# Kernel optimization log

Hardware: AMD Instinct MI355X
Metric: run time of the kernel (lower is better)

The kernel has to match this reference:

```python
import jax, jax.numpy as jnp
import numpy as np

B, N, E, D = 4, 4096, 4096, 128
NEG_SLOPE = 0.01
BN_EPS = 1e-5


def setup_inputs() -> dict:
    key = jax.random.key(0)
    ks = jax.random.split(key, 8)
    return {
        "incident_mat": (jax.random.uniform(ks[0], (B, N, E)) < 0.01).astype(jnp.float32),
        "degree_v": jax.random.normal(ks[1], (B, N, N), jnp.float32) * 0.01,
        "degree_e": jax.random.normal(ks[2], (B, E, E), jnp.float32) * 0.01,
        "x": jax.random.normal(ks[3], (B, N, D), jnp.float32),
        "e_masks": jax.random.randint(ks[4], (B, E), 0, 2, jnp.int32),
        "mlp_W": jax.random.normal(ks[5], (D, D), jnp.float32) / np.sqrt(D),
        "mlp_b": jnp.zeros((D,), jnp.float32),
        "theta_att": jax.random.normal(ks[6], (D, 1), jnp.float32) / np.sqrt(D),
        "eps": jax.random.uniform(ks[7], (1,), jnp.float32),
        "bn_gamma": jnp.ones((D,), jnp.float32),
        "bn_beta": jnp.zeros((D,), jnp.float32),
        "bn_mean": jnp.zeros((D,), jnp.float32),
        "bn_var": jnp.ones((D,), jnp.float32),
    }


def reference(incident_mat, degree_v, degree_e, x, e_masks, mlp_W, mlp_b,
              theta_att, eps, bn_gamma, bn_beta, bn_mean, bn_var):
    # MLP (num_mlp_layers=1 -> single Linear)
    x_w = x @ mlp_W + mlp_b                      # [B,N,D]
    Ht = jnp.swapaxes(incident_mat, 1, 2)        # [B,E,N]
    ht_x_w = Ht @ x_w                            # [B,E,D]
    # attention logits per hyperedge
    ht_x_theta = (Ht @ (x @ theta_att))[..., 0]  # [B,E]
    scores = jnp.where(e_masks == 0, -jnp.inf, ht_x_theta)
    attn = jax.nn.softmax(scores, axis=1)        # [B,E]
    # diag_embed + bmm == elementwise row scaling
    h1 = attn[..., None] * ht_x_w                # [B,E,D]
    h1 = incident_mat @ h1                       # [B,N,D]
    h1 = degree_v @ h1                           # [B,N,D]
    h1 = Ht @ h1                                 # [B,E,D]
    h1 = degree_e @ h1                           # [B,E,D]
    h = h1 + eps * ht_x_w                        # [B,E,D]
    h = incident_mat @ h                         # [B,N,D]
    h = jnp.where(h >= 0, h, NEG_SLOPE * h)      # leaky_relu; dropout=identity (eval)
    # BatchNorm1d over channels (inference mode)
    h = (h - bn_mean) / jnp.sqrt(bn_var + BN_EPS) * bn_gamma + bn_beta
    return h
```

## Files before the change

### kernel.cpp

```cpp
#include <hip/hip_runtime.h>


typedef __bf16 bf16;
typedef bf16 bf16x8 __attribute__((ext_vector_type(8)));
typedef float f32x4 __attribute__((ext_vector_type(4)));
typedef unsigned long long u64;

#define LDK 72
#define SWZ(r, c) ((c) ^ ((((r) >> 3) & 7) << 3))
#define CAP 192

union BPack { bf16 h[2]; unsigned int u; };
static __device__ __forceinline__ bf16 tob(float f) { return (bf16)f; }

__global__ __launch_bounds__(256) void mlp_k(const float* __restrict__ x,
                                             const float* __restrict__ W,
                                             const float* __restrict__ bias,
                                             const float* __restrict__ theta,
                                             float* __restrict__ xw,
                                             float* __restrict__ xt) {
    __shared__ float Ws[32][128];
    __shared__ float xs[32][128];
    const int t = threadIdx.x;
    const long r0 = (long)blockIdx.x * 32;

    for (int i = t * 4; i < 4096; i += 1024)
        *(float4*)&xs[i >> 7][i & 127] = *(const float4*)&x[r0 * 128 + i];

    const int d = t & 127;
    const int rg = (t >> 7) * 16;
    float acc[16];
#pragma unroll
    for (int r = 0; r < 16; ++r) acc[r] = 0.f;

    for (int kk = 0; kk < 128; kk += 32) {
        __syncthreads();
        for (int i = t * 4; i < 4096; i += 1024)
            *(float4*)&Ws[i >> 7][i & 127] =
                *(const float4*)&W[(kk + (i >> 7)) * 128 + (i & 127)];
        __syncthreads();
        for (int k = 0; k < 32; ++k) {
            float w = Ws[k][d];
#pragma unroll
            for (int r = 0; r < 16; ++r) acc[r] += xs[rg + r][kk + k] * w;
        }
    }
    const float bd = bias[d];
#pragma unroll
    for (int r = 0; r < 16; ++r)
        xw[(r0 + rg + r) * 128 + d] = acc[r] + bd;

    if (t < 32) {
        float s = 0.f;
        for (int k = 0; k < 128; ++k) s += xs[t][k] * theta[k];
        xt[r0 + t] = s;
    }
}

__global__ __launch_bounds__(256) void bmask2_k(const float* __restrict__ inc,
                                                u64* __restrict__ rowmask) {
    const int b = blockIdx.y;
    const int n = blockIdx.x * 4 + (threadIdx.x >> 6);
    const int l = threadIdx.x & 63;
    const float* p = inc + ((long)b << 24) + (long)n * 4096 + l * 64;
    u64 w = 0;
#pragma unroll
    for (int j = 0; j < 16; ++j) {
        const float4 v = *(const float4*)(p + j * 4);
        w |= (u64)(v.x != 0.f ? 1u : 0u) << (4 * j);
        w |= (u64)(v.y != 0.f ? 1u : 0u) << (4 * j + 1);
        w |= (u64)(v.z != 0.f ? 1u : 0u) << (4 * j + 2);
        w |= (u64)(v.w != 0.f ? 1u : 0u) << (4 * j + 3);
    }
    rowmask[((long)b * 4096 + n) * 64 + l] = w;
}

__global__ void btrans_k(const u64* __restrict__ rowmask, u64* __restrict__ colmask) {
    const int tn = blockIdx.x, te = blockIdx.y, b = blockIdx.z;
    const int l = threadIdx.x;
    __shared__ u64 w[64];
    w[l] = rowmask[((long)b * 4096 + tn * 64 + l) * 64 + te];
    __syncthreads();
    u64 o = 0;
#pragma unroll 8
    for (int j = 0; j < 64; ++j) o |= ((w[j] >> l) & 1ull) << j;
    colmask[((long)b * 4096 + te * 64 + l) * 64 + tn] = o;
}

__global__ __launch_bounds__(256) void lists_k(const u64* __restrict__ mask,
                                               ushort* __restrict__ idx,
                                               int* __restrict__ cnts) {
    const int b = blockIdx.y;
    const int r = blockIdx.x * 4 + (threadIdx.x >> 6);
    const int l = threadIdx.x & 63;
    u64 m = mask[((long)b * 4096 + r) * 64 + l];
    const int pc = __popcll(m);
    int pre = pc;
#pragma unroll
    for (int o = 1; o < 64; o <<= 1) {
        int t = __shfl_up(pre, o);
        if (l >= o) pre += t;
    }
    const int total = __shfl(pre, 63);
    if (l == 63) cnts[b * 4096 + r] = total;
    ushort* op = idx + ((long)b * 4096 + r) * CAP;
    int k = pre - pc;
    while (m) {
        const int bit = __builtin_ctzll(m);
        m &= m - 1;
        if (k < CAP) op[k] = (ushort)(l * 64 + bit);
        ++k;
    }
}

__global__ void softmax_k(const float* __restrict__ sc, const int* __restrict__ mask,
                          float* __restrict__ attn) {
    const int b = blockIdx.x, t = threadIdx.x;
    __shared__ float red[1024];
    const float* sb = sc + b * 4096;
    const int* mb = mask + b * 4096;

    float mx = -1e30f;
    for (int e = t; e < 4096; e += 1024)
        if (mb[e] != 0) mx = fmaxf(mx, sb[e]);
    red[t] = mx;
    __syncthreads();
    for (int st = 512; st > 0; st >>= 1) {
        if (t < st) red[t] = fmaxf(red[t], red[t + st]);
        __syncthreads();
    }
    mx = red[0];
    __syncthreads();

    float sum = 0.f;
    for (int e = t; e < 4096; e += 1024)
        if (mb[e] != 0) sum += expf(sb[e] - mx);
    red[t] = sum;
    __syncthreads();
    for (int st = 512; st > 0; st >>= 1) {
        if (t < st) red[t] += red[t + st];
        __syncthreads();
    }
    const float inv = 1.f / red[0];
    for (int e = t; e < 4096; e += 1024)
        attn[b * 4096 + e] = (mb[e] != 0) ? expf(sb[e] - mx) * inv : 0.f;
}

__global__ __launch_bounds__(256) void pairsum_k(const float* __restrict__ P,
                                                 float* __restrict__ O) {
    const long i4 = (long)blockIdx.x * 256 + threadIdx.x;
    float4 a = ((const float4*)P)[i4];
    float4 c = ((const float4*)P)[i4 + 524288];
    a.x += c.x; a.y += c.y; a.z += c.z; a.w += c.w;
    ((float4*)O)[i4] = a;
}

template <bool SCALE, bool ADDEPS, bool HXT, bool EPI>
__global__ __launch_bounds__(256) void gatherE_k(
    const ushort* __restrict__ idx, const int* __restrict__ cnts,
    const u64* __restrict__ mask, const float* __restrict__ src,
    const float* __restrict__ src2, const float* __restrict__ attn,
    const float* __restrict__ xt, const float* __restrict__ epsp,
    const float* __restrict__ bng, const float* __restrict__ bnb,
    const float* __restrict__ bnm, const float* __restrict__ bnv,
    float* __restrict__ out, float* __restrict__ hxt) {
    const int bid = blockIdx.x;
    const int slot = bid & 7;
    const int b = slot >> 1;
    const int chunk = (bid >> 3) * 2 + (slot & 1);
    const int r = chunk * 4 + (threadIdx.x >> 6);
    const int l = threadIdx.x & 63;
    const long rowid = (long)b * 4096 + r;
    const int cnt = cnts[rowid];
    const ushort* ip = idx + rowid * CAP;
    const float* S = src + (long)b * 524288;
    const float* S2 = ADDEPS ? (src2 + (long)b * 524288) : nullptr;
    const float* ab = attn + (long)b * 4096;
    const float* xb = xt + (long)b * 4096;
    const float eps_v = ADDEPS ? epsp[0] : 0.f;
    const int c0 = 2 * l;

    float a0x = 0.f, a0y = 0.f, a1x = 0.f, a1y = 0.f;
    float a2x = 0.f, a2y = 0.f, a3x = 0.f, a3y = 0.f;
    float hacc = 0.f;

    auto edge1 = [&](int e) {
        float2 v = *(const float2*)(S + (long)e * 128 + c0);
        if (ADDEPS) {
            float2 u = *(const float2*)(S2 + (long)e * 128 + c0);
            v.x += eps_v * u.x; v.y += eps_v * u.y;
        }
        if (SCALE) {
            const float s = ab[e];
            v.x *= s; v.y *= s;
        }
        if (HXT) hacc += xb[e];
        a0x += v.x; a0y += v.y;
    };

    const int n = cnt < CAP ? cnt : CAP;
    int i = 0;
    for (; i + 4 <= n; i += 4) {
        const int e0 = ip[i], e1 = ip[i + 1], e2 = ip[i + 2], e3 = ip[i + 3];
        float2 v0 = *(const float2*)(S + (long)e0 * 128 + c0);
        float2 v1 = *(const float2*)(S + (long)e1 * 128 + c0);
        float2 v2 = *(const float2*)(S + (long)e2 * 128 + c0);
        float2 v3 = *(const float2*)(S + (long)e3 * 128 + c0);
        if (ADDEPS) {
            float2 u0 = *(const float2*)(S2 + (long)e0 * 128 + c0);
            float2 u1 = *(const float2*)(S2 + (long)e1 * 128 + c0);
            float2 u2 = *(const float2*)(S2 + (long)e2 * 128 + c0);
            float2 u3 = *(const float2*)(S2 + (long)e3 * 128 + c0);
            v0.x += eps_v * u0.x; v0.y += eps_v * u0.y;
            v1.x += eps_v * u1.x; v1.y += eps_v * u1.y;
            v2.x += eps_v * u2.x; v2.y += eps_v * u2.y;
            v3.x += eps_v * u3.x; v3.y += eps_v * u3.y;
        }
        if (SCALE) {
            const float s0 = ab[e0], s1 = ab[e1], s2 = ab[e2], s3 = ab[e3];
            v0.x *= s0; v0.y *= s0; v1.x *= s1; v1.y *= s1;
            v2.x *= s2; v2.y *= s2; v3.x *= s3; v3.y *= s3;
        }
        if (HXT) hacc += (xb[e0] + xb[e1]) + (xb[e2] + xb[e3]);
        a0x += v0.x; a0y += v0.y; a1x += v1.x; a1y += v1.y;
        a2x += v2.x; a2y += v2.y; a3x += v3.x; a3y += v3.y;
    }
    for (; i < n; ++i) edge1(ip[i]);

    if (cnt > CAP) {
        const u64 wrd = mask[rowid * 64 + l];
        int seen = 0;
        for (int wi = 0; wi < 64; ++wi) {
            u64 m = __shfl(wrd, wi);
            const int pc = __popcll(m);
            if (seen + pc > CAP) {
                int tk = CAP - seen;
                if (tk < 0) tk = 0;
                for (int t = 0; t < tk; ++t) m &= m - 1;
                while (m) {
                    const int bit = __builtin_ctzll(m);
                    m &= m - 1;
                    edge1((wi << 6) + bit);
                }
            }
            seen += pc;
        }
    }

    float ax = (a0x + a1x) + (a2x + a3x);
    float ay = (a0y + a1y) + (a2y + a3y);
    if (EPI) {
        float t0 = (ax >= 0.f) ? ax : 0.01f * ax;
        float t1 = (ay >= 0.f) ? ay : 0.01f * ay;
        ax = (t0 - bnm[c0]) * rsqrtf(bnv[c0] + 1e-5f) * bng[c0] + bnb[c0];
        ay = (t1 - bnm[c0 + 1]) * rsqrtf(bnv[c0 + 1] + 1e-5f) * bng[c0 + 1] + bnb[c0 + 1];
    }
    *(float2*)&out[(long)b * 524288 + (long)r * 128 + c0] = (float2){ax, ay};
    if (HXT && l == 0) hxt[rowid] = hacc;
}

template <int KS>
__global__ __launch_bounds__(1024, 4) void gemm_dense(
    const float* __restrict__ A, const float* __restrict__ Bsrc,
    float* __restrict__ P) {
    __shared__ __align__(16) bf16 As[2][128][LDK];
    __shared__ __align__(16) bf16 Bs[2][128][LDK];

    const int tid = threadIdx.x;
    const int bid = blockIdx.x;
    const int slot = bid & 7;
    const int b = slot >> 1;
    const int sub = (bid >> 3) * 2 + (slot & 1);
    const int ksi = sub % KS;
    const int m0 = (sub / KS) * 128;
    constexpr int KCH = 4096 / KS;
    const int kbeg = ksi * KCH, kend = kbeg + KCH;
    const long Aoff = (long)b << 24;
    const long Boff = (long)b * 524288;

    const int wave = tid >> 6, lane = tid & 63;
    const int lr = lane & 15, kb = lane >> 4;
    const int wm = (wave >> 2) * 32, wn = (wave & 3) * 32;

    const int ar = tid >> 3, ak = (tid & 7) * 8;
    const int bd4 = (tid & 31) * 4, bk2 = (tid >> 5) * 2;

    const float* Abase = A + Aoff + (long)(m0 + ar) * 4096 + ak;
    const float* Bbase = Bsrc + Boff + (long)bk2 * 128 + bd4;

    f32x4 acc[2][2];
#pragma unroll
    for (int mf = 0; mf < 2; ++mf)
#pragma unroll
        for (int nf = 0; nf < 2; ++nf) acc[mf][nf] = (f32x4){0.f, 0.f, 0.f, 0.f};

    float4 pa0A, pa1A, pb0A, pb1A;
    float4 pa0B, pa1B, pb0B, pb1B;

#define GLOAD(S, kk)                                                        \
    {                                                                       \
        const float* ga = Abase + (kk);                                     \
        pa0##S = *(const float4*)ga;                                        \
        pa1##S = *(const float4*)(ga + 4);                                  \
        const float* gb = Bbase + (long)(kk) * 128;                         \
        pb0##S = *(const float4*)gb;                                        \
        pb1##S = *(const float4*)(gb + 128);                                \
    }

#define STAGE(S, bu)                                                        \
    {                                                                       \
        bf16x8 p;                                                           \
        p[0] = tob(pa0##S.x); p[1] = tob(pa0##S.y); p[2] = tob(pa0##S.z); p[3] = tob(pa0##S.w); \
        p[4] = tob(pa1##S.x); p[5] = tob(pa1##S.y); p[6] = tob(pa1##S.z); p[7] = tob(pa1##S.w); \
        *(bf16x8*)&As[bu][ar][SWZ(ar, ak)] = p;                             \
        float va[4] = {pb0##S.x, pb0##S.y, pb0##S.z, pb0##S.w};             \
        float vb[4] = {pb1##S.x, pb1##S.y, pb1##S.z, pb1##S.w};             \
        _Pragma("unroll")                                                   \
        for (int j = 0; j < 4; ++j) {                                       \
            BPack q; q.h[0] = tob(va[j]); q.h[1] = tob(vb[j]);              \
            *(unsigned int*)&Bs[bu][bd4 + j][SWZ(bd4 + j, bk2)] = q.u;      \
        }                                                                   \
    }

#define MFMA_STEP(bu)                                                       \
    {                                                                       \
        _Pragma("unroll")                                                   \
        for (int ks = 0; ks < 2; ++ks) {                                    \
            const int ka = ks * 32 + kb * 8;                                \
            bf16x8 af[2], bfr[2];                                           \
            _Pragma("unroll")                                               \
            for (int mf = 0; mf < 2; ++mf) {                                \
                const int rA = wm + mf * 16 + lr;                           \
                af[mf] = *(const bf16x8*)&As[bu][rA][SWZ(rA, ka)];          \
            }                                                               \
            _Pragma("unroll")                                               \
            for (int nf = 0; nf < 2; ++nf) {                                \
                const int rB = wn + nf * 16 + lr;                           \
                bfr[nf] = *(const bf16x8*)&Bs[bu][rB][SWZ(rB, ka)];         \
            }                                                               \
            _Pragma("unroll")                                               \
            for (int mf = 0; mf < 2; ++mf)                                  \
                _Pragma("unroll")                                           \
                for (int nf = 0; nf < 2; ++nf)                              \
                    acc[mf][nf] = __builtin_amdgcn_mfma_f32_16x16x32_bf16(  \
                        af[mf], bfr[nf], acc[mf][nf], 0, 0, 0);             \
        }                                                                   \
    }

    GLOAD(A, kbeg);
    GLOAD(B, kbeg + 64);
    STAGE(A, 0);
    __syncthreads();

    for (int kk = kbeg; kk < kend; kk += 128) {
        MFMA_STEP(0);
        STAGE(B, 1);
        if (kk + 128 < kend) GLOAD(A, kk + 128);
        __syncthreads();
        MFMA_STEP(1);
        if (kk + 128 < kend) {
            STAGE(A, 0);
            if (kk + 192 < kend) GLOAD(B, kk + 192);
            __syncthreads();
        }
    }
#undef GLOAD
#undef STAGE
#undef MFMA_STEP

    float* Cp = P + (long)(ksi * 4 + b) * 524288;
#pragma unroll
    for (int mf = 0; mf < 2; ++mf) {
        const int rb = m0 + wm + mf * 16 + kb * 4;
#pragma unroll
        for (int nf = 0; nf < 2; ++nf) {
            const int col = wn + nf * 16 + lr;
#pragma unroll
            for (int i = 0; i < 4; ++i)
                Cp[(long)(rb + i) * 128 + col] = acc[mf][nf][i];
        }
    }
}

template <int KS>
static void run_all(const float* incident, const float* degree_v, const float* degree_e,
                    const float* x, const int* e_masks, const float* mlp_W,
                    const float* mlp_b, const float* theta, const float* epsp,
                    const float* bng, const float* bnb, const float* bnm,
                    const float* bnv, float* out, float* ws, hipStream_t stream) {
    float* xw  = ws;
    float* hxw = ws + 2097152;
    float* t1  = ws + 4194304;
    float* Pd  = ws + 6291456;
    float* Psum = Pd + (long)KS * 2097152;
    float* tail = Psum + 2097152;
    u64* rowmask = (u64*)tail;
    u64* colmask = rowmask + 1048576;
    ushort* rowidx = (ushort*)(colmask + 1048576);
    ushort* colidx = rowidx + 16384 * CAP;
    int* rowcnt = (int*)(colidx + 16384 * CAP);
    int* colcnt = rowcnt + 16384;
    float* xt  = (float*)(colcnt + 16384);
    float* hxt = xt + 16384;
    float* att = hxt + 16384;

    mlp_k<<<512, 256, 0, stream>>>(x, mlp_W, mlp_b, theta, xw, xt);
    bmask2_k<<<dim3(1024, 4), 256, 0, stream>>>(incident, rowmask);
    btrans_k<<<dim3(64, 64, 4), 64, 0, stream>>>(rowmask, colmask);
    lists_k<<<dim3(1024, 4), 256, 0, stream>>>(rowmask, rowidx, rowcnt);
    lists_k<<<dim3(1024, 4), 256, 0, stream>>>(colmask, colidx, colcnt);

    gatherE_k<false, false, true, false><<<4096, 256, 0, stream>>>(
        colidx, colcnt, colmask, xw, nullptr, att, xt, nullptr,
        nullptr, nullptr, nullptr, nullptr, hxw, hxt);
    softmax_k<<<4, 1024, 0, stream>>>(hxt, e_masks, att);
    gatherE_k<true, false, false, false><<<4096, 256, 0, stream>>>(
        rowidx, rowcnt, rowmask, hxw, nullptr, att, xt, nullptr,
        nullptr, nullptr, nullptr, nullptr, t1, nullptr);
    gemm_dense<KS><<<32 * KS * 4, 1024, 0, stream>>>(degree_v, t1, Pd);
    const float* g4src = Pd;
    if (KS == 2) { pairsum_k<<<2048, 256, 0, stream>>>(Pd, Psum); g4src = Psum; }
    gatherE_k<false, false, false, false><<<4096, 256, 0, stream>>>(
        colidx, colcnt, colmask, g4src, nullptr, att, xt, nullptr,
        nullptr, nullptr, nullptr, nullptr, t1, nullptr);
    gemm_dense<KS><<<32 * KS * 4, 1024, 0, stream>>>(degree_e, t1, Pd);
    const float* g6src = Pd;
    if (KS == 2) { pairsum_k<<<2048, 256, 0, stream>>>(Pd, Psum); g6src = Psum; }
    gatherE_k<false, true, false, true><<<4096, 256, 0, stream>>>(
        rowidx, rowcnt, rowmask, g6src, hxw, att, xt, epsp,
        bng, bnb, bnm, bnv, out, nullptr);
}

extern "C" void kernel_launch(void* const* d_in, const int* in_sizes, int n_in,
                              void* d_out, int out_size, void* d_ws, size_t ws_size,
                              hipStream_t stream) {
    const float* incident = (const float*)d_in[0];
    const float* degree_v = (const float*)d_in[1];
    const float* degree_e = (const float*)d_in[2];
    const float* x        = (const float*)d_in[3];
    const int*   e_masks  = (const int*)d_in[4];
    const float* mlp_W    = (const float*)d_in[5];
    const float* mlp_b    = (const float*)d_in[6];
    const float* theta    = (const float*)d_in[7];
    const float* epsp     = (const float*)d_in[8];
    const float* bng      = (const float*)d_in[9];
    const float* bnb      = (const float*)d_in[10];
    const float* bnm      = (const float*)d_in[11];
    const float* bnv      = (const float*)d_in[12];
    float* out = (float*)d_out;
    float* ws = (float*)d_ws;

    if (ws_size >= 95000000ull)
        run_all<2>(incident, degree_v, degree_e, x, e_masks, mlp_W, mlp_b, theta,
                   epsp, bng, bnb, bnm, bnv, out, ws, stream);
    else
        run_all<1>(incident, degree_v, degree_e, x, e_masks, mlp_W, mlp_b, theta,
                   epsp, bng, bnb, bnm, bnv, out, ws, stream);
}
```

Baseline: 431.1 us.

## Fuse row-list build into mask kernel and hoist scaling and eps out of gathers

Builds the row index lists inside the mask kernel, so the separate lists pass and its rowmask reread go away. The per-edge attention scaling and eps*hxw add move out of the gather kernels into dense elementwise passes (a new scale kernel and a pairsum kernel that also adds eps), so every gather reads a single source with no extra per-element loads. The gather loop now loads eight indices at once as a vector, keeps eight independent accumulators and prefetches the next index batch. The cost is extra launches and a larger workspace; the threshold for the split-K path is raised to match, which could change which path runs for some workspace sizes.

```diff
diff --git a/kernel.cpp b/kernel.cpp
--- a/kernel.cpp
+++ b/kernel.cpp
@@ -5,6 +5,8 @@
 typedef bf16 bf16x8 __attribute__((ext_vector_type(8)));
 typedef float f32x4 __attribute__((ext_vector_type(4)));
 typedef unsigned long long u64;
+typedef unsigned short u16;
+typedef u16 u16x8 __attribute__((ext_vector_type(8)));
 
 #define LDK 72
 #define SWZ(r, c) ((c) ^ ((((r) >> 3) & 7) << 3))
@@ -57,8 +59,10 @@
     }
 }
 
-__global__ __launch_bounds__(256) void bmask2_k(const float* __restrict__ inc,
-                                                u64* __restrict__ rowmask) {
+__global__ __launch_bounds__(256) void bmask_lists_k(const float* __restrict__ inc,
+                                                     u64* __restrict__ rowmask,
+                                                     u16* __restrict__ idx,
+                                                     int* __restrict__ cnts) {
     const int b = blockIdx.y;
     const int n = blockIdx.x * 4 + (threadIdx.x >> 6);
     const int l = threadIdx.x & 63;
@@ -72,7 +76,26 @@
         w |= (u64)(v.z != 0.f ? 1u : 0u) << (4 * j + 2);
         w |= (u64)(v.w != 0.f ? 1u : 0u) << (4 * j + 3);
     }
-    rowmask[((long)b * 4096 + n) * 64 + l] = w;
+    const long rowid = (long)b * 4096 + n;
+    rowmask[rowid * 64 + l] = w;
+
+    const int pc = __popcll(w);
+    int pre = pc;
+#pragma unroll
+    for (int o = 1; o < 64; o <<= 1) {
+        int t = __shfl_up(pre, o);
+        if (l >= o) pre += t;
+    }
+    if (l == 63) cnts[rowid] = pre;
+    u16* op = idx + rowid * CAP;
+    int k = pre - pc;
+    u64 m = w;
+    while (m) {
+        const int bit = __builtin_ctzll(m);
+        m &= m - 1;
+        if (k < CAP) op[k] = (u16)(l * 64 + bit);
+        ++k;
+    }
 }
 
 __global__ void btrans_k(const u64* __restrict__ rowmask, u64* __restrict__ colmask) {
@@ -88,7 +111,7 @@
 }
 
 __global__ __launch_bounds__(256) void lists_k(const u64* __restrict__ mask,
-                                               ushort* __restrict__ idx,
+                                               u16* __restrict__ idx,
                                                int* __restrict__ cnts) {
     const int b = blockIdx.y;
     const int r = blockIdx.x * 4 + (threadIdx.x >> 6);
@@ -101,14 +124,13 @@
         int t = __shfl_up(pre, o);
         if (l >= o) pre += t;
     }
-    const int total = __shfl(pre, 63);
-    if (l == 63) cnts[b * 4096 + r] = total;
-    ushort* op = idx + ((long)b * 4096 + r) * CAP;
+    if (l == 63) cnts[b * 4096 + r] = pre;
+    u16* op = idx + ((long)b * 4096 + r) * CAP;
     int k = pre - pc;
     while (m) {
         const int bit = __builtin_ctzll(m);
         m &= m - 1;
-        if (k < CAP) op[k] = (ushort)(l * 64 + bit);
+        if (k < CAP) op[k] = (u16)(l * 64 + bit);
         ++k;
     }
 }
@@ -146,21 +168,40 @@
         attn[b * 4096 + e] = (mb[e] != 0) ? expf(sb[e] - mx) * inv : 0.f;
 }
 
+__global__ __launch_bounds__(256) void scale_k(const float* __restrict__ hxw,
+                                               const float* __restrict__ att,
+                                               float* __restrict__ outp) {
+    const long i4 = (long)blockIdx.x * 256 + threadIdx.x;
+    float4 v = ((const float4*)hxw)[i4];
+    const float s = att[i4 >> 5];
+    v.x *= s; v.y *= s; v.z *= s; v.w *= s;
+    ((float4*)outp)[i4] = v;
+}
+
+template <int KSP, bool EPS>
 __global__ __launch_bounds__(256) void pairsum_k(const float* __restrict__ P,
+                                                 const float* __restrict__ H,
+                                                 const float* __restrict__ epsp,
                                                  float* __restrict__ O) {
     const long i4 = (long)blockIdx.x * 256 + threadIdx.x;
     float4 a = ((const float4*)P)[i4];
-    float4 c = ((const float4*)P)[i4 + 524288];
-    a.x += c.x; a.y += c.y; a.z += c.z; a.w += c.w;
+    if (KSP == 2) {
+        float4 c = ((const float4*)P)[i4 + 524288];
+        a.x += c.x; a.y += c.y; a.z += c.z; a.w += c.w;
+    }
+    if (EPS) {
+        const float e = epsp[0];
+        float4 h = ((const float4*)H)[i4];
+        a.x += e * h.x; a.y += e * h.y; a.z += e * h.z; a.w += e * h.w;
+    }
     ((float4*)O)[i4] = a;
 }
 
-template <bool SCALE, bool ADDEPS, bool HXT, bool EPI>
+template <bool HXT, bool EPI>
 __global__ __launch_bounds__(256) void gatherE_k(
-    const ushort* __restrict__ idx, const int* __restrict__ cnts,
+    const u16* __restrict__ idx, const int* __restrict__ cnts,
     const u64* __restrict__ mask, const float* __restrict__ src,
-    const float* __restrict__ src2, const float* __restrict__ attn,
-    const float* __restrict__ xt, const float* __restrict__ epsp,
+    const float* __restrict__ xt,
     const float* __restrict__ bng, const float* __restrict__ bnb,
     const float* __restrict__ bnm, const float* __restrict__ bnv,
     float* __restrict__ out, float* __restrict__ hxt) {
@@ -172,60 +213,51 @@
     const int l = threadIdx.x & 63;
     const long rowid = (long)b * 4096 + r;
     const int cnt = cnts[rowid];
-    const ushort* ip = idx + rowid * CAP;
+    const u16* ip = idx + rowid * CAP;
     const float* S = src + (long)b * 524288;
-    const float* S2 = ADDEPS ? (src2 + (long)b * 524288) : nullptr;
-    const float* ab = attn + (long)b * 4096;
     const float* xb = xt + (long)b * 4096;
-    const float eps_v = ADDEPS ? epsp[0] : 0.f;
     const int c0 = 2 * l;
 
-    float a0x = 0.f, a0y = 0.f, a1x = 0.f, a1y = 0.f;
-    float a2x = 0.f, a2y = 0.f, a3x = 0.f, a3y = 0.f;
+    float ax0 = 0.f, ax1 = 0.f, ax2 = 0.f, ax3 = 0.f;
+    float ax4 = 0.f, ax5 = 0.f, ax6 = 0.f, ax7 = 0.f;
+    float ay0 = 0.f, ay1 = 0.f, ay2 = 0.f, ay3 = 0.f;
+    float ay4 = 0.f, ay5 = 0.f, ay6 = 0.f, ay7 = 0.f;
     float hacc = 0.f;
-
-    auto edge1 = [&](int e) {
-        float2 v = *(const float2*)(S + (long)e * 128 + c0);
-        if (ADDEPS) {
-            float2 u = *(const float2*)(S2 + (long)e * 128 + c0);
-            v.x += eps_v * u.x; v.y += eps_v * u.y;
-        }
-        if (SCALE) {
-            const float s = ab[e];
-            v.x *= s; v.y *= s;
-        }
-        if (HXT) hacc += xb[e];
-        a0x += v.x; a0y += v.y;
-    };
 
     const int n = cnt < CAP ? cnt : CAP;
     int i = 0;
-    for (; i + 4 <= n; i += 4) {
-        const int e0 = ip[i], e1 = ip[i + 1], e2 = ip[i + 2], e3 = ip[i + 3];
-        float2 v0 = *(const float2*)(S + (long)e0 * 128 + c0);
-        float2 v1 = *(const float2*)(S + (long)e1 * 128 + c0);
-        float2 v2 = *(const float2*)(S + (long)e2 * 128 + c0);
-        float2 v3 = *(const float2*)(S + (long)e3 * 128 + c0);
-        if (ADDEPS) {
-            float2 u0 = *(const float2*)(S2 + (long)e0 * 128 + c0);
-            float2 u1 = *(const float2*)(S2 + (long)e1 * 128 + c0);
-            float2 u2 = *(const float2*)(S2 + (long)e2 * 128 + c0);
-            float2 u3 = *(const float2*)(S2 + (long)e3 * 128 + c0);
-            v0.x += eps_v * u0.x; v0.y += eps_v * u0.y;
-            v1.x += eps_v * u1.x; v1.y += eps_v * u1.y;
-            v2.x += eps_v * u2.x; v2.y += eps_v * u2.y;
-            v3.x += eps_v * u3.x; v3.y += eps_v * u3.y;
+    if (n >= 8) {
+        u16x8 ia = *(const u16x8*)ip;
+        for (; i + 8 <= n; i += 8) {
+            const int e0 = ia[0], e1 = ia[1], e2 = ia[2], e3 = ia[3];
+            const int e4 = ia[4], e5 = ia[5], e6 = ia[6], e7 = ia[7];
+            const float2 v0 = *(const float2*)(S + (long)e0 * 128 + c0);
+            const float2 v1 = *(const float2*)(S + (long)e1 * 128 + c0);
+            const float2 v2 = *(const float2*)(S + (long)e2 * 128 + c0);
+            const float2 v3 = *(const float2*)(S + (long)e3 * 128 + c0);
+            const float2 v4 = *(const float2*)(S + (long)e4 * 128 + c0);
+            const float2 v5 = *(const float2*)(S + (long)e5 * 128 + c0);
+            const float2 v6 = *(const float2*)(S + (long)e6 * 128 + c0);
+            const float2 v7 = *(const float2*)(S + (long)e7 * 128 + c0);
+            const bool more = (i + 16 <= n);
+            u16x8 ib;
+            if (more) ib = *(const u16x8*)(ip + i + 8);
+            if (HXT)
+                hacc += ((xb[e0] + xb[e1]) + (xb[e2] + xb[e3])) +
+                        ((xb[e4] + xb[e5]) + (xb[e6] + xb[e7]));
+            ax0 += v0.x; ay0 += v0.y; ax1 += v1.x; ay1 += v1.y;
+            ax2 += v2.x; ay2 += v2.y; ax3 += v3.x; ay3 += v3.y;
+            ax4 += v4.x; ay4 += v4.y; ax5 += v5.x; ay5 += v5.y;
+            ax6 += v6.x; ay6 += v6.y; ax7 += v7.x; ay7 += v7.y;
+            if (more) ia = ib;
         }
-        if (SCALE) {
-            const float s0 = ab[e0], s1 = ab[e1], s2 = ab[e2], s3 = ab[e3];
-            v0.x *= s0; v0.y *= s0; v1.x *= s1; v1.y *= s1;
-            v2.x *= s2; v2.y *= s2; v3.x *= s3; v3.y *= s3;
-        }
-        if (HXT) hacc += (xb[e0] + xb[e1]) + (xb[e2] + xb[e3]);
-        a0x += v0.x; a0y += v0.y; a1x += v1.x; a1y += v1.y;
-        a2x += v2.x; a2y += v2.y; a3x += v3.x; a3y += v3.y;
-    }
-    for (; i < n; ++i) edge1(ip[i]);
+    }
+    for (; i < n; ++i) {
+        const int e = ip[i];
+        const float2 v = *(const float2*)(S + (long)e * 128 + c0);
+        if (HXT) hacc += xb[e];
+        ax0 += v.x; ay0 += v.y;
+    }
 
     if (cnt > CAP) {
         const u64 wrd = mask[rowid * 64 + l];
@@ -240,15 +272,18 @@
                 while (m) {
                     const int bit = __builtin_ctzll(m);
                     m &= m - 1;
-                    edge1((wi << 6) + bit);
+                    const int e = (wi << 6) + bit;
+                    const float2 v = *(const float2*)(S + (long)e * 128 + c0);
+                    if (HXT) hacc += xb[e];
+                    ax0 += v.x; ay0 += v.y;
                 }
             }
             seen += pc;
         }
     }
 
-    float ax = (a0x + a1x) + (a2x + a3x);
-    float ay = (a0y + a1y) + (a2y + a3y);
+    float ax = ((ax0 + ax1) + (ax2 + ax3)) + ((ax4 + ax5) + (ax6 + ax7));
+    float ay = ((ay0 + ay1) + (ay2 + ay3)) + ((ay4 + ay5) + (ay6 + ay7));
     if (EPI) {
         float t0 = (ax >= 0.f) ? ax : 0.01f * ax;
         float t1 = (ay >= 0.f) ? ay : 0.01f * ay;
@@ -388,16 +423,17 @@
                     const float* mlp_b, const float* theta, const float* epsp,
                     const float* bng, const float* bnb, const float* bnm,
                     const float* bnv, float* out, float* ws, hipStream_t stream) {
-    float* xw  = ws;
-    float* hxw = ws + 2097152;
-    float* t1  = ws + 4194304;
-    float* Pd  = ws + 6291456;
-    float* Psum = Pd + (long)KS * 2097152;
-    float* tail = Psum + 2097152;
+    float* xw    = ws;
+    float* hxw   = ws + 2097152;
+    float* hxw_s = ws + 4194304;
+    float* t1    = ws + 6291456;
+    float* Pd    = ws + 8388608;
+    float* Psum  = Pd + (long)KS * 2097152;
+    float* tail  = Psum + 2097152;
     u64* rowmask = (u64*)tail;
     u64* colmask = rowmask + 1048576;
-    ushort* rowidx = (ushort*)(colmask + 1048576);
-    ushort* colidx = rowidx + 16384 * CAP;
+    u16* rowidx = (u16*)(colmask + 1048576);
+    u16* colidx = rowidx + 16384 * CAP;
     int* rowcnt = (int*)(colidx + 16384 * CAP);
     int* colcnt = rowcnt + 16384;
     float* xt  = (float*)(colcnt + 16384);
@@ -405,30 +441,27 @@
     float* att = hxt + 16384;
 
     mlp_k<<<512, 256, 0, stream>>>(x, mlp_W, mlp_b, theta, xw, xt);
-    bmask2_k<<<dim3(1024, 4), 256, 0, stream>>>(incident, rowmask);
+    bmask_lists_k<<<dim3(1024, 4), 256, 0, stream>>>(incident, rowmask, rowidx, rowcnt);
     btrans_k<<<dim3(64, 64, 4), 64, 0, stream>>>(rowmask, colmask);
-    lists_k<<<dim3(1024, 4), 256, 0, stream>>>(rowmask, rowidx, rowcnt);
     lists_k<<<dim3(1024, 4), 256, 0, stream>>>(colmask, colidx, colcnt);
 
-    gatherE_k<false, false, true, false><<<4096, 256, 0, stream>>>(
-        colidx, colcnt, colmask, xw, nullptr, att, xt, nullptr,
-        nullptr, nullptr, nullptr, nullptr, hxw, hxt);
+    gatherE_k<true, false><<<4096, 256, 0, stream>>>(
+        colidx, colcnt, colmask, xw, xt, nullptr, nullptr, nullptr, nullptr,
+        hxw, hxt);
     softmax_k<<<4, 1024, 0, stream>>>(hxt, e_masks, att);
-    gatherE_k<true, false, false, false><<<4096, 256, 0, stream>>>(
-        rowidx, rowcnt, rowmask, hxw, nullptr, att, xt, nullptr,
-        nullptr, nullptr, nullptr, nullptr, t1, nullptr);
+    scale_k<<<2048, 256, 0, stream>>>(hxw, att, hxw_s);
+    gatherE_k<false, false><<<4096, 256, 0, stream>>>(
+        rowidx, rowcnt, rowmask, hxw_s, xt, nullptr, nullptr, nullptr, nullptr,
+        t1, nullptr);
     gemm_dense<KS><<<32 * KS * 4, 1024, 0, stream>>>(degree_v, t1, Pd);
-    const float* g4src = Pd;
-    if (KS == 2) { pairsum_k<<<2048, 256, 0, stream>>>(Pd, Psum); g4src = Psum; }
-    gatherE_k<false, false, false, false><<<4096, 256, 0, stream>>>(
-        colidx, colcnt, colmask, g4src, nullptr, att, xt, nullptr,
-        nullptr, nullptr, nullptr, nullptr, t1, nullptr);
+    pairsum_k<KS, false><<<2048, 256, 0, stream>>>(Pd, nullptr, nullptr, Psum);
+    gatherE_k<false, false><<<4096, 256, 0, stream>>>(
+        colidx, colcnt, colmask, Psum, xt, nullptr, nullptr, nullptr, nullptr,
+        t1, nullptr);
     gemm_dense<KS><<<32 * KS * 4, 1024, 0, stream>>>(degree_e, t1, Pd);
-    const float* g6src = Pd;
-    if (KS == 2) { pairsum_k<<<2048, 256, 0, stream>>>(Pd, Psum); g6src = Psum; }
-    gatherE_k<false, true, false, true><<<4096, 256, 0, stream>>>(
-        rowidx, rowcnt, rowmask, g6src, hxw, att, xt, epsp,
-        bng, bnb, bnm, bnv, out, nullptr);
+    pairsum_k<KS, true><<<2048, 256, 0, stream>>>(Pd, hxw, epsp, Psum);
+    gatherE_k<false, true><<<4096, 256, 0, stream>>>(
+        rowidx, rowcnt, rowmask, Psum, xt, bng, bnb, bnm, bnv, out, nullptr);
 }
 
 extern "C" void kernel_launch(void* const* d_in, const int* in_sizes, int n_in,
@@ -450,7 +483,7 @@
     float* out = (float*)d_out;
     float* ws = (float*)d_ws;
 
-    if (ws_size >= 95000000ull)
+    if (ws_size >= 110000000ull)
         run_all<2>(incident, degree_v, degree_e, x, e_masks, mlp_W, mlp_b, theta,
                    epsp, bng, bnb, bnm, bnv, out, ws, stream);
     else
```

Result: faster. 404.0 us (-6.3%).
